# Performance work log

Measured on AMD Instinct MI355X. Metric: run time of the kernel, lower is better.

## Reference

```python
import jax, jax.numpy as jnp
import numpy as np

N = 8192       # nodes
IN_F = 512     # in_features
OUT_F = 256    # out_features


def setup_inputs() -> dict:
    key = jax.random.key(0)
    k1, k2, k3, k4 = jax.random.split(key, 4)
    # xavier_uniform-like scales for params
    w_scale = 1.414 * (6.0 / (IN_F + OUT_F)) ** 0.5
    a_scale = 1.414 * (6.0 / (2 * OUT_F + 1)) ** 0.5
    x = jax.random.normal(k1, (N, IN_F), jnp.float32)
    W = jax.random.uniform(k2, (IN_F, OUT_F), jnp.float32, -w_scale, w_scale)
    a = jax.random.uniform(k3, (2 * OUT_F, 1), jnp.float32, -a_scale, a_scale)
    adj = jax.random.randint(k4, (N, N), 0, 2, jnp.int32)
    return {"x": x, "W": W, "a": a, "adj": adj}


def reference(x, W, a, adj):
    # h = x @ W : [N, OUT_F]
    h = x @ W
    f = W.shape[1]
    a1, a2 = a[:f], a[f:]          # each [OUT_F, 1]
    # Original builds a_input[i,j] = concat(h_i, h_j) then matmuls with a.
    # Equivalent decomposition: e[i,j] = h_i . a1 + h_j . a2
    e = (h @ a1) + (h @ a2).T      # [N, N]
    neg = jnp.float32(-9e15)
    attention = jnp.where(adj > 0, e, neg)   # no softmax in the original
    h_prime = attention @ h        # [N, OUT_F]
    return h_prime
```

## Files before the change

kernel.cpp:

```cpp
#include <hip/hip_runtime.h>


#define NEG_BIG (-9000000000000000.0f)
#define POS_BIG (9000000000000000.0f)

typedef __bf16 bf16x8 __attribute__((ext_vector_type(8)));
typedef float f32x16 __attribute__((ext_vector_type(16)));

static __device__ __forceinline__ unsigned short f2bf(float f) {
  unsigned u = __builtin_bit_cast(unsigned, f);
  u = u + 0x7FFFu + ((u >> 16) & 1u);
  return (unsigned short)(u >> 16);
}
static __device__ __forceinline__ float bfbits2f(unsigned hi16) {
  return __builtin_bit_cast(float, hi16 << 16);
}
static __device__ __forceinline__ unsigned pk2(float a, float b) {
  return (unsigned)f2bf(a) | ((unsigned)f2bf(b) << 16);
}
static __device__ __forceinline__ unsigned m2(int a, int b) {
  return (unsigned)(a + (b << 16)) * 0x3F80u;
}
static __device__ __forceinline__ bf16x8 asbf(int4 q) {
  return __builtin_bit_cast(bf16x8, q);
}
static __device__ __forceinline__ f32x16 mfma(bf16x8 a, int4 b, f32x16 c) {
  return __builtin_amdgcn_mfma_f32_32x32x16_bf16(a, asbf(b), c, 0, 0, 0);
}

__global__ void k1a_wt(const float* __restrict__ W, unsigned short* __restrict__ WT,
                       float* __restrict__ T) {
  const int i = blockIdx.x * 256 + threadIdx.x;
  const int k = i >> 8, n = i & 255;
  WT[n * 512 + k] = f2bf(W[i]);
  if (blockIdx.x == 0) T[threadIdx.x] = 0.f;
}

__global__ __launch_bounds__(256) void k1b_h(const float* __restrict__ x,
    const unsigned short* __restrict__ WT, unsigned short* __restrict__ hP) {
  __shared__ unsigned short XS[64 * 264];
  const int t = threadIdx.x;
  const int mt = blockIdx.x;
  const int m0 = mt << 5;
  const int row = t >> 3, c7 = t & 7;
  const float* xr = x + (size_t)(m0 + row) * 512 + c7 * 4;
  const int gb = c7 >> 1, off = (t & 1) * 4;
#pragma unroll
  for (int j = 0; j < 16; ++j) {
    float4 v = *(const float4*)(xr + 32 * j);
    *(uint2*)&XS[(gb + 4 * j) * 264 + row * 8 + off] =
        make_uint2(pk2(v.x, v.y), pk2(v.z, v.w));
  }
  __syncthreads();
  const int w = t >> 6, l = t & 63, l31 = l & 31, lh = l >> 5;
  f32x16 acc0, acc1;
  for (int i = 0; i < 16; ++i) { acc0[i] = 0.f; acc1[i] = 0.f; }
  const int nt0 = w * 2;
  const unsigned short* w0 = WT + (size_t)(nt0 * 32 + l31) * 512 + lh * 8;
  const unsigned short* w1 = w0 + 32 * 512;
  const char* XB = (const char*)XS + lh * 528 + l31 * 16;
#pragma unroll 4
  for (int ks = 0; ks < 32; ++ks) {
    bf16x8 Af = *(const bf16x8*)(XB + ks * 1056);
    int4 b0 = *(const int4*)(w0 + ks * 16);
    int4 b1 = *(const int4*)(w1 + ks * 16);
    acc0 = mfma(Af, b0, acc0);
    acc1 = mfma(Af, b1, acc1);
  }
#pragma unroll
  for (int reg = 0; reg < 16; ++reg) {
    const int mm = (reg & 3) + 8 * (reg >> 2) + 4 * lh;
    hP[(size_t)mt * 8192 + (nt0 * 32 + l31) * 32 + mm] = f2bf(acc0[reg]);
    hP[(size_t)mt * 8192 + ((nt0 + 1) * 32 + l31) * 32 + mm] = f2bf(acc1[reg]);
  }
}

__global__ __launch_bounds__(256) void k2_colsum(const unsigned short* __restrict__ hP,
                                                 float* __restrict__ T) {
  const int t = threadIdx.x;
  const int b = blockIdx.x;
  const int4* p = (const int4*)(hP + (size_t)b * 8192 + t * 32);
  int4 q0 = p[0], q1 = p[1], q2 = p[2], q3 = p[3];
  float s = 0.f;
  const unsigned* u0 = (const unsigned*)&q0;
  const unsigned* u1 = (const unsigned*)&q1;
  const unsigned* u2 = (const unsigned*)&q2;
  const unsigned* u3 = (const unsigned*)&q3;
#pragma unroll
  for (int i = 0; i < 4; ++i) {
    s += bfbits2f(u0[i] & 0xFFFFu) + bfbits2f(u0[i] >> 16);
    s += bfbits2f(u1[i] & 0xFFFFu) + bfbits2f(u1[i] >> 16);
    s += bfbits2f(u2[i] & 0xFFFFu) + bfbits2f(u2[i] >> 16);
    s += bfbits2f(u3[i] & 0xFFFFu) + bfbits2f(u3[i] >> 16);
  }
  atomicAdd(&T[t], s);
}

__global__ void k2b_init(const float* __restrict__ T, float* __restrict__ out) {
  const int i = blockIdx.x * 256 + threadIdx.x;
  const int n4 = (i & 63) * 4;
  float4 tv = *(const float4*)(T + n4);
  float4 o;
  o.x = NEG_BIG * tv.x; o.y = NEG_BIG * tv.y;
  o.z = NEG_BIG * tv.z; o.w = NEG_BIG * tv.w;
  ((float4*)out)[i] = o;
}

template<int MODE>
__global__ __launch_bounds__(256, 2) void k3_att(const int* __restrict__ adj,
    const unsigned short* __restrict__ hP, float* __restrict__ outp) {
  __shared__ unsigned short S[4][2][4 * 512];
  const int t = threadIdx.x, blk = blockIdx.x;
  const int s = blk & 7;
  const int rg = blk >> 3;
  const int w = t >> 6, l = t & 63, l31 = l & 31, lh = l >> 5;
  const int rt = rg * 2 + (w >> 1);
  const int nh = w & 1;

  const int* aB = adj + (size_t)(rt * 64 + (l >> 3)) * 8192 + s * 1024 + (l & 7) * 4;
  const int woff = ((l & 7) >> 1) * 512 + (l >> 3) * 8 + (l & 1) * 4;
  unsigned short* const Sw0 = &S[w][0][0];
  unsigned short* const Sw1 = &S[w][1][0];
  const unsigned short* hB = hP + (size_t)(s * 32) * 8192
                              + (size_t)(nh * 128 + l31) * 32 + lh * 8;
  const int fr = lh * 1024 + l31 * 16;

  f32x16 acc[2][4];
#pragma unroll
  for (int mt = 0; mt < 2; ++mt)
#pragma unroll
    for (int nt = 0; nt < 4; ++nt)
#pragma unroll
      for (int i = 0; i < 16; ++i) acc[mt][nt][i] = 0.f;

  int4 gA[8], Bv[8];

#define ALOAD(it)                                                           \
  _Pragma("unroll")                                                         \
  for (int q = 0; q < 8; ++q)                                               \
    gA[q] = *(const int4*)(aB + (size_t)q * 8 * 8192 + (it) * 32);
#define APACK(buf)                                                          \
  _Pragma("unroll")                                                         \
  for (int q = 0; q < 8; ++q)                                               \
    *(uint2*)&buf[woff + q * 64] =                                          \
        make_uint2(m2(gA[q].x, gA[q].y), m2(gA[q].z, gA[q].w));
#define BLOAD(it)                                                           \
  {                                                                         \
    const unsigned short* hb = hB + (size_t)(it) * 8192;                    \
    _Pragma("unroll")                                                       \
    for (int ks = 0; ks < 2; ++ks)                                          \
      _Pragma("unroll")                                                     \
      for (int nt = 0; nt < 4; ++nt)                                        \
        Bv[ks * 4 + nt] = *(const int4*)(hb + nt * 1024 + ks * 16);         \
  }
#define COMP(buf)                                                           \
  {                                                                         \
    const char* Ab = (const char*)(buf) + fr;                               \
    _Pragma("unroll")                                                       \
    for (int ks = 0; ks < 2; ++ks) {                                        \
      bf16x8 A0 = *(const bf16x8*)(Ab + ks * 2048);                         \
      bf16x8 A1 = *(const bf16x8*)(Ab + ks * 2048 + 512);                   \
      _Pragma("unroll")                                                     \
      for (int nt = 0; nt < 4; ++nt) {                                      \
        acc[0][nt] = mfma(A0, Bv[ks * 4 + nt], acc[0][nt]);                 \
        acc[1][nt] = mfma(A1, Bv[ks * 4 + nt], acc[1][nt]);                 \
      }                                                                     \
    }                                                                       \
  }

  ALOAD(0)
  APACK(Sw0)
  ALOAD(1)

#pragma unroll 1
  for (int it = 0; it < 32; ++it) {
    unsigned short* const Scur = (it & 1) ? Sw1 : Sw0;
    unsigned short* const Snxt = (it & 1) ? Sw0 : Sw1;
    BLOAD(it)
    if (it + 1 < 32) { APACK(Snxt) }
    if (it + 2 < 32) { ALOAD(it + 2) }
    COMP(Scur)
  }
#undef ALOAD
#undef APACK
#undef BLOAD
#undef COMP

#pragma unroll
  for (int mt = 0; mt < 2; ++mt)
#pragma unroll
    for (int nt = 0; nt < 4; ++nt) {
      const int nn = nh * 128 + nt * 32 + l31;
#pragma unroll
      for (int reg = 0; reg < 16; ++reg) {
        const int rr = rt * 64 + mt * 32 + (reg & 3) + 8 * (reg >> 2) + 4 * lh;
        if (MODE == 0) {
          outp[(size_t)s * 2097152 + (size_t)rr * 256 + nn] = acc[mt][nt][reg];
        } else {
          atomicAdd(outp + (size_t)rr * 256 + nn, POS_BIG * acc[mt][nt][reg]);
        }
      }
    }
}

__global__ __launch_bounds__(256) void k4_reduce(const float* __restrict__ P,
    const float* __restrict__ T, float* __restrict__ out) {
  const int i = blockIdx.x * 256 + threadIdx.x;
  float4 tv = *(const float4*)(T + (i & 63) * 4);
  const float4* P4 = (const float4*)P;
  float sx = 0.f, sy = 0.f, sz = 0.f, sw = 0.f;
#pragma unroll
  for (int sp = 0; sp < 8; ++sp) {
    float4 v = P4[(size_t)sp * 524288 + i];
    sx += v.x; sy += v.y; sz += v.z; sw += v.w;
  }
  float4 o;
  o.x = POS_BIG * sx + NEG_BIG * tv.x;
  o.y = POS_BIG * sy + NEG_BIG * tv.y;
  o.z = POS_BIG * sz + NEG_BIG * tv.z;
  o.w = POS_BIG * sw + NEG_BIG * tv.w;
  ((float4*)out)[i] = o;
}

extern "C" void kernel_launch(void* const* d_in, const int* in_sizes, int n_in,
                              void* d_out, int out_size, void* d_ws, size_t ws_size,
                              hipStream_t stream) {
  const float* x = (const float*)d_in[0];
  const float* W = (const float*)d_in[1];
  const int* adj = (const int*)d_in[3];
  float* out = (float*)d_out;
  char* ws = (char*)d_ws;
  unsigned short* WT = (unsigned short*)(ws);
  unsigned short* hP = (unsigned short*)(ws + (1 << 20));
  float* T = (float*)(ws + (6 << 20));
  float* P = (float*)(ws + (8 << 20));

  const bool fit = ws_size >= ((size_t)(8 << 20) + (size_t)64 * 1024 * 1024);

  k1a_wt<<<512, 256, 0, stream>>>(W, WT, T);
  k1b_h<<<256, 256, 0, stream>>>(x, WT, hP);
  k2_colsum<<<256, 256, 0, stream>>>(hP, T);
  if (fit) {
    k3_att<0><<<512, 256, 0, stream>>>(adj, hP, P);
    k4_reduce<<<2048, 256, 0, stream>>>(P, T, out);
  } else {
    k2b_init<<<2048, 256, 0, stream>>>(T, out);
    k3_att<1><<<512, 256, 0, stream>>>(adj, hP, out);
  }
}
```

Baseline: 461.3 us.

## Pre-pack adjacency into transposed bitmask and expand bits directly to MFMA operands

Adds a pre-pass kernel that reads the int32 adjacency matrix once and writes a transposed 1-bit-per-entry mask. The attention GEMM then loads single bytes and expands them in registers into bf16 A operands. This drops the LDS staging, the double-buffered int4 adjacency loads and the packing step from the main loop. The full 256MB adjacency read still happens in the new pre-pass, and the main loop now issues many scattered byte loads and does extra ALU work for the bit expansion.

```diff
diff --git a/kernel.cpp b/kernel.cpp
--- a/kernel.cpp
+++ b/kernel.cpp
@@ -18,14 +18,60 @@
 static __device__ __forceinline__ unsigned pk2(float a, float b) {
   return (unsigned)f2bf(a) | ((unsigned)f2bf(b) << 16);
 }
-static __device__ __forceinline__ unsigned m2(int a, int b) {
-  return (unsigned)(a + (b << 16)) * 0x3F80u;
-}
 static __device__ __forceinline__ bf16x8 asbf(int4 q) {
   return __builtin_bit_cast(bf16x8, q);
 }
 static __device__ __forceinline__ f32x16 mfma(bf16x8 a, int4 b, f32x16 c) {
   return __builtin_amdgcn_mfma_f32_32x32x16_bf16(a, asbf(b), c, 0, 0, 0);
+}
+static __device__ __forceinline__ bf16x8 expand8(unsigned b) {
+  union { unsigned w[4]; bf16x8 f; } r;
+  r.w[0] = ((b & 1u)        | ((b & 2u)   << 15)) * 0x3F80u;
+  r.w[1] = (((b >> 2) & 1u) | ((b & 8u)   << 13)) * 0x3F80u;
+  r.w[2] = (((b >> 4) & 1u) | ((b & 32u)  << 11)) * 0x3F80u;
+  r.w[3] = (((b >> 6) & 1u) | ((b & 128u) << 9))  * 0x3F80u;
+  return r.f;
+}
+
+__global__ __launch_bounds__(256, 2) void k0_bits(const int* __restrict__ adj,
+                                                  unsigned char* __restrict__ bitT) {
+  __shared__ unsigned char LT[1024 * 20];
+  const int t = threadIdx.x;
+  const int rb = blockIdx.x;
+  const int* base = adj + (size_t)rb * 16 * 8192 + t * 32;
+  unsigned c[4] = {0u, 0u, 0u, 0u};
+#pragma unroll
+  for (int rr = 0; rr < 16; ++rr) {
+    const int4* p = (const int4*)(base + (size_t)rr * 8192);
+    int4 q[8];
+#pragma unroll
+    for (int k = 0; k < 8; ++k) q[k] = p[k];
+#pragma unroll
+    for (int i = 0; i < 4; ++i) {
+      int4 u = q[2 * i], v = q[2 * i + 1];
+      unsigned by = (u.x & 1) | ((u.y & 1) << 1) | ((u.z & 1) << 2) | ((u.w & 1) << 3)
+                  | ((v.x & 1) << 4) | ((v.y & 1) << 5) | ((v.z & 1) << 6) | ((v.w & 1) << 7);
+      c[i] |= by << ((rr & 3) * 8);
+    }
+    if ((rr & 3) == 3) {
+#pragma unroll
+      for (int i = 0; i < 4; ++i) {
+        *(unsigned*)&LT[(t * 4 + i) * 20 + (rr & ~3)] = c[i];
+        c[i] = 0u;
+      }
+    }
+  }
+  __syncthreads();
+#pragma unroll
+  for (int jc = 0; jc < 4; ++jc) {
+    const int j8 = jc * 256 + t;
+    int4 v;
+    v.x = *(const int*)&LT[j8 * 20];
+    v.y = *(const int*)&LT[j8 * 20 + 4];
+    v.z = *(const int*)&LT[j8 * 20 + 8];
+    v.w = *(const int*)&LT[j8 * 20 + 12];
+    *(int4*)(bitT + (size_t)j8 * 8192 + rb * 16) = v;
+  }
 }
 
 __global__ void k1a_wt(const float* __restrict__ W, unsigned short* __restrict__ WT,
@@ -107,9 +153,8 @@
 }
 
 template<int MODE>
-__global__ __launch_bounds__(256, 2) void k3_att(const int* __restrict__ adj,
+__global__ __launch_bounds__(256, 2) void k3_att(const unsigned char* __restrict__ bitT,
     const unsigned short* __restrict__ hP, float* __restrict__ outp) {
-  __shared__ unsigned short S[4][2][4 * 512];
   const int t = threadIdx.x, blk = blockIdx.x;
   const int s = blk & 7;
   const int rg = blk >> 3;
@@ -117,13 +162,9 @@
   const int rt = rg * 2 + (w >> 1);
   const int nh = w & 1;
 
-  const int* aB = adj + (size_t)(rt * 64 + (l >> 3)) * 8192 + s * 1024 + (l & 7) * 4;
-  const int woff = ((l & 7) >> 1) * 512 + (l >> 3) * 8 + (l & 1) * 4;
-  unsigned short* const Sw0 = &S[w][0][0];
-  unsigned short* const Sw1 = &S[w][1][0];
+  const unsigned char* bq = bitT + (size_t)(s * 128 + lh) * 8192 + rt * 64 + l31;
   const unsigned short* hB = hP + (size_t)(s * 32) * 8192
                               + (size_t)(nh * 128 + l31) * 32 + lh * 8;
-  const int fr = lh * 1024 + l31 * 16;
 
   f32x16 acc[2][4];
 #pragma unroll
@@ -133,17 +174,13 @@
 #pragma unroll
       for (int i = 0; i < 16; ++i) acc[mt][nt][i] = 0.f;
 
-  int4 gA[8], Bv[8];
-
-#define ALOAD(it)                                                           \
+  int4 Bv[8];
+  unsigned cb[4], nb[4];
+
+#define BYTELOAD(dst, it)                                                   \
   _Pragma("unroll")                                                         \
-  for (int q = 0; q < 8; ++q)                                               \
-    gA[q] = *(const int4*)(aB + (size_t)q * 8 * 8192 + (it) * 32);
-#define APACK(buf)                                                          \
-  _Pragma("unroll")                                                         \
-  for (int q = 0; q < 8; ++q)                                               \
-    *(uint2*)&buf[woff + q * 64] =                                          \
-        make_uint2(m2(gA[q].x, gA[q].y), m2(gA[q].z, gA[q].w));
+  for (int mk = 0; mk < 4; ++mk)                                            \
+    dst[mk] = bq[(size_t)((it) * 4 + (mk & 1) * 2) * 8192 + (mk >> 1) * 32];
 #define BLOAD(it)                                                           \
   {                                                                         \
     const unsigned short* hb = hB + (size_t)(it) * 8192;                    \
@@ -153,38 +190,28 @@
       for (int nt = 0; nt < 4; ++nt)                                        \
         Bv[ks * 4 + nt] = *(const int4*)(hb + nt * 1024 + ks * 16);         \
   }
-#define COMP(buf)                                                           \
-  {                                                                         \
-    const char* Ab = (const char*)(buf) + fr;                               \
-    _Pragma("unroll")                                                       \
-    for (int ks = 0; ks < 2; ++ks) {                                        \
-      bf16x8 A0 = *(const bf16x8*)(Ab + ks * 2048);                         \
-      bf16x8 A1 = *(const bf16x8*)(Ab + ks * 2048 + 512);                   \
-      _Pragma("unroll")                                                     \
-      for (int nt = 0; nt < 4; ++nt) {                                      \
-        acc[0][nt] = mfma(A0, Bv[ks * 4 + nt], acc[0][nt]);                 \
-        acc[1][nt] = mfma(A1, Bv[ks * 4 + nt], acc[1][nt]);                 \
-      }                                                                     \
-    }                                                                       \
-  }
-
-  ALOAD(0)
-  APACK(Sw0)
-  ALOAD(1)
+
+  BYTELOAD(cb, 0)
 
 #pragma unroll 1
   for (int it = 0; it < 32; ++it) {
-    unsigned short* const Scur = (it & 1) ? Sw1 : Sw0;
-    unsigned short* const Snxt = (it & 1) ? Sw0 : Sw1;
     BLOAD(it)
-    if (it + 1 < 32) { APACK(Snxt) }
-    if (it + 2 < 32) { ALOAD(it + 2) }
-    COMP(Scur)
-  }
-#undef ALOAD
-#undef APACK
+    if (it + 1 < 32) { BYTELOAD(nb, it + 1) }
+#pragma unroll
+    for (int ks = 0; ks < 2; ++ks) {
+      bf16x8 A0 = expand8(cb[ks]);
+      bf16x8 A1 = expand8(cb[2 + ks]);
+#pragma unroll
+      for (int nt = 0; nt < 4; ++nt) {
+        acc[0][nt] = mfma(A0, Bv[ks * 4 + nt], acc[0][nt]);
+        acc[1][nt] = mfma(A1, Bv[ks * 4 + nt], acc[1][nt]);
+      }
+    }
+#pragma unroll
+    for (int mk = 0; mk < 4; ++mk) cb[mk] = nb[mk];
+  }
+#undef BYTELOAD
 #undef BLOAD
-#undef COMP
 
 #pragma unroll
   for (int mt = 0; mt < 2; ++mt)
@@ -233,18 +260,20 @@
   unsigned short* WT = (unsigned short*)(ws);
   unsigned short* hP = (unsigned short*)(ws + (1 << 20));
   float* T = (float*)(ws + (6 << 20));
-  float* P = (float*)(ws + (8 << 20));
-
-  const bool fit = ws_size >= ((size_t)(8 << 20) + (size_t)64 * 1024 * 1024);
-
+  unsigned char* bitT = (unsigned char*)(ws + (16 << 20));
+  float* P = (float*)(ws + (32 << 20));
+
+  const bool fit = ws_size >= ((size_t)(32 << 20) + (size_t)64 * 1024 * 1024);
+
+  k0_bits<<<512, 256, 0, stream>>>(adj, bitT);
   k1a_wt<<<512, 256, 0, stream>>>(W, WT, T);
   k1b_h<<<256, 256, 0, stream>>>(x, WT, hP);
   k2_colsum<<<256, 256, 0, stream>>>(hP, T);
   if (fit) {
-    k3_att<0><<<512, 256, 0, stream>>>(adj, hP, P);
+    k3_att<0><<<512, 256, 0, stream>>>(bitT, hP, P);
     k4_reduce<<<2048, 256, 0, stream>>>(P, T, out);
   } else {
     k2b_init<<<2048, 256, 0, stream>>>(T, out);
-    k3_att<1><<<512, 256, 0, stream>>>(adj, hP, out);
-  }
-}
+    k3_att<1><<<512, 256, 0, stream>>>(bitT, hP, out);
+  }
+}
```

Result: slower. 525.7 us (+14.0%).
